# Kernel tuning notes

Measured on AMD Instinct MI355X. Metric: run time of the kernel, lower is better.

## Reference

```python
import jax, jax.numpy as jnp
import numpy as np
import math

FACTOR = 1

def setup_inputs() -> dict:
    key = jax.random.key(0)
    k1, k2, k3 = jax.random.split(key, 3)
    B, L, H, E = 32, 1024, 8, 64
    return {
        "queries": jax.random.normal(k1, (B, L, H, E), dtype=jnp.float32),
        "keys": jax.random.normal(k2, (B, L, H, E), dtype=jnp.float32),
        "values": jax.random.normal(k3, (B, L, H, E), dtype=jnp.float32),
        "attn_mask": 0,
    }


def reference(queries, keys, values, attn_mask):
    # queries/keys/values: [B, L, H, E] (S == L so no pad/truncate needed)
    B, L, H, E = queries.shape
    q = jnp.transpose(queries, (0, 2, 3, 1))  # [B,H,E,L]
    k = jnp.transpose(keys, (0, 2, 3, 1))
    v = jnp.transpose(values, (0, 2, 3, 1))   # [B,H,D,L]

    # FFT cross-correlation
    q_fft = jnp.fft.rfft(q, axis=-1)
    k_fft = jnp.fft.rfft(k, axis=-1)
    corr = jnp.fft.irfft(q_fft * jnp.conj(k_fft), n=L, axis=-1)  # [B,H,E,L]

    # top-k delay selection (global over batch, as in source)
    top_k = min(int(FACTOR * math.log(L)), L // 4, 32)  # static: 6
    mean_value = corr.mean(axis=(1, 2))                 # [B,L]
    weights, indices = jax.lax.top_k(mean_value.mean(axis=0), top_k)  # [k]
    tmp_corr = jax.nn.softmax(weights)                  # [k]

    # weighted circular-shift aggregation: roll(v, -indices[i]) summed with tmp_corr[i]
    pos = (jnp.arange(L)[None, :] + indices[:, None]) % L  # [k,L]
    patterns = v[:, :, :, pos]                              # [B,H,D,k,L]
    delays_agg = jnp.einsum('k,bhdkl->bhdl', tmp_corr, patterns)

    return jnp.transpose(delays_agg, (0, 3, 1, 2))  # [B,L,H,D]
```

## Files before the change

kernel.cpp:

```cpp
#include <hip/hip_runtime.h>
#include <math.h>

#define L_SEQ 1024
#define TOPK 6
#define SSTR 1057
#define NFBLK 2048

__device__ constexpr float TW32R[16] = {
  1.f, 0.98078528f, 0.92387953f, 0.83146961f, 0.70710678f, 0.55557023f,
  0.38268343f, 0.19509032f, 0.f, -0.19509032f, -0.38268343f, -0.55557023f,
  -0.70710678f, -0.83146961f, -0.92387953f, -0.98078528f};
__device__ constexpr float TW32I[16] = {
  0.f, -0.19509032f, -0.38268343f, -0.55557023f, -0.70710678f, -0.83146961f,
  -0.92387953f, -0.98078528f, -1.f, -0.98078528f, -0.92387953f, -0.83146961f,
  -0.70710678f, -0.55557023f, -0.38268343f, -0.19509032f};

#define FFTSTAGE(M, H, SH)                                                \
  _Pragma("unroll")                                                       \
  for (int k_ = 0; k_ < 32; k_ += (M)) {                                  \
    _Pragma("unroll")                                                     \
    for (int t_ = 0; t_ < (H); ++t_) {                                    \
      const int a_ = k_ + t_, b_ = a_ + (H);                              \
      const int m_ = t_ << (SH);                                          \
      float vr_, vi_;                                                     \
      if (m_ == 0)      { vr_ = zr[b_]; vi_ = zi[b_]; }                   \
      else if (m_ == 8) { vr_ = zi[b_]; vi_ = -zr[b_]; }                  \
      else {                                                              \
        vr_ = zr[b_] * TW32R[m_] - zi[b_] * TW32I[m_];                    \
        vi_ = zr[b_] * TW32I[m_] + zi[b_] * TW32R[m_];                    \
      }                                                                   \
      zr[b_] = zr[a_] - vr_; zi[b_] = zi[a_] - vi_;                       \
      zr[a_] += vr_;         zi[a_] += vi_;                               \
    }                                                                     \
  }

__global__ __launch_bounds__(256, 2) void fft_spec_kernel(
    const float* __restrict__ q, const float* __restrict__ k,
    float* __restrict__ partial)
{
  __shared__ float pr[8 * SSTR];
  __shared__ float pim[8 * SSTR];

  const int tid = threadIdx.x;
  const int bid = blockIdx.x;

  const int wq  = bid >> 3;
  const int xcd = bid & 7;
  const int octet = (wq & 1) | (((wq >> 1) & 3) << 1);
  const int h = (wq >> 3) & 7;
  const int b = (xcd << 2) | (wq >> 6);

  const float* qb = q + (size_t)b * 524288 + h * 64 + octet * 8;
  const float* kb = k + (size_t)b * 524288 + h * 64 + octet * 8;

  {
    const int ep = (tid & 1) * 4;
    const int lb = tid >> 1;
    const int col0 = (lb & 31) * 33 + (lb >> 5);
    #pragma unroll
    for (int it = 0; it < 8; ++it) {
      const int l = it * 128 + lb;
      const float4 qv = *(const float4*)(qb + (size_t)l * 512 + ep);
      const float4 kv = *(const float4*)(kb + (size_t)l * 512 + ep);
      const int col = col0 + it * 4;
      pr[(ep + 0) * SSTR + col] = qv.x;
      pr[(ep + 1) * SSTR + col] = qv.y;
      pr[(ep + 2) * SSTR + col] = qv.z;
      pr[(ep + 3) * SSTR + col] = qv.w;
      pim[(ep + 0) * SSTR + col] = kv.x;
      pim[(ep + 1) * SSTR + col] = kv.y;
      pim[(ep + 2) * SSTR + col] = kv.z;
      pim[(ep + 3) * SSTR + col] = kv.w;
    }
  }
  __syncthreads();

  const int s = tid >> 5;
  const int i = tid & 31;
  constexpr int BR[32] = {0,16,8,24,4,20,12,28,2,18,10,26,6,22,14,30,
                          1,17,9,25,5,21,13,29,3,19,11,27,7,23,15,31};
  const float astep = (float)i * 6.13592315e-03f;
  float zr[32], zi[32];

  {
    const int rowbase = s * SSTR + i * 33;
    #pragma unroll
    for (int p = 0; p < 32; ++p) {
      zr[p] = pr[rowbase + BR[p]];
      zi[p] = pim[rowbase + BR[p]];
    }
    FFTSTAGE(2, 1, 4) FFTSTAGE(4, 2, 3) FFTSTAGE(8, 4, 2)
    FFTSTAGE(16, 8, 1) FFTSTAGE(32, 16, 0)
    #pragma unroll
    for (int k2 = 0; k2 < 32; ++k2) {
      if (k2 == 0) {
        pr[rowbase]  = zr[0];
        pim[rowbase] = zi[0];
      } else {
        float sa, ca;
        __sincosf(astep * (float)k2, &sa, &ca);
        pr[rowbase + k2]  = zr[k2] * ca + zi[k2] * sa;
        pim[rowbase + k2] = zi[k2] * ca - zr[k2] * sa;
      }
    }
  }
  __syncthreads();

  const int j = i;
  #pragma unroll
  for (int p = 0; p < 32; ++p) {
    zr[p] = pr[s * SSTR + BR[p] * 33 + j];
    zi[p] = pim[s * SSTR + BR[p] * 33 + j];
  }
  __syncthreads();
  FFTSTAGE(2, 1, 4) FFTSTAGE(4, 2, 3) FFTSTAGE(8, 4, 2)
  FFTSTAGE(16, 8, 1) FFTSTAGE(32, 16, 0)

  {
    const int t64 = tid & 63;
    const int pl = (t64 & 32) | ((32 - j) & 31);
    #pragma unroll
    for (int k1 = 0; k1 < 32; ++k1) {
      float xr = __shfl(zr[31 - k1], pl, 64);
      float xi = __shfl(zi[31 - k1], pl, 64);
      if (j == 0) { xr = zr[(32 - k1) & 31]; xi = zi[(32 - k1) & 31]; }
      const float ar = zr[k1], ai = zi[k1];
      pr [s * SSTR + j * 33 + k1] = 0.5f  * (ar * xi + ai * xr);
      pim[s * SSTR + j * 33 + k1] = 0.25f * (ar * ar + ai * ai
                                             - xr * xr - xi * xi);
    }
  }
  __syncthreads();

  #pragma unroll
  for (int u = 0; u < 8; ++u) {
    const int bin = u * 256 + tid;
    const int bb = bin & 1023;
    const int jj = bb & 31, kk = bb >> 5;
    const float* pl_ = (u >= 4) ? pim : pr;
    float acc = 0.f;
    #pragma unroll
    for (int s2 = 0; s2 < 8; ++s2) acc += pl_[s2 * SSTR + jj * 33 + kk];
    partial[(size_t)bid * 2048 + bin] = acc;
  }
}

__global__ __launch_bounds__(256) void spec_reduce(
    const float* __restrict__ partial, float* __restrict__ S)
{
  const int t = threadIdx.x;
  const int b64 = t & 63, rc = t >> 6;
  const int v = blockIdx.x * 64 + b64;
  float acc = 0.f;
  for (int rr = rc * 512; rr < rc * 512 + 512; ++rr)
    acc += partial[(size_t)rr * 2048 + v];
  __shared__ float sm[4][65];
  sm[rc][b64] = acc;
  __syncthreads();
  if (t < 64)
    S[v] = sm[0][t] + sm[1][t] + sm[2][t] + sm[3][t];
}

__global__ __launch_bounds__(256) void corr_kernel(
    const float* __restrict__ S, float* __restrict__ c)
{
  __shared__ float sm[8][33];
  const int t = threadIdx.x;
  const int tau = blockIdx.x * 32 + (t & 31);
  const int jc = t >> 5;
  float acc = 0.f;
  #pragma unroll 4
  for (int jj = 0; jj < 128; ++jj) {
    const int j = jc * 128 + jj;
    float s_, c_;
    __sincosf((float)((j * tau) & 1023) * 6.13592315e-03f, &s_, &c_);
    acc += S[j] * c_ - S[1024 + j] * s_;
  }
  sm[jc][t & 31] = acc;
  __syncthreads();
  if (t < 32) {
    float r = 0.f;
    #pragma unroll
    for (int g = 0; g < 8; ++g) r += sm[g][t];
    c[blockIdx.x * 32 + t] = r * (1.0f / 16777216.0f);
  }
}

__global__ __launch_bounds__(256) void topk_kernel(
    const float* __restrict__ c, int* __restrict__ idx_out,
    float* __restrict__ w_out)
{
  __shared__ float vals[L_SEQ];
  __shared__ float rv[256];
  __shared__ int ri[256];
  __shared__ float topv[TOPK];
  __shared__ int topi[TOPK];
  const int tid = threadIdx.x;
  for (int i = tid; i < L_SEQ; i += 256) vals[i] = c[i];
  __syncthreads();

  for (int kk = 0; kk < TOPK; ++kk) {
    float bv = -INFINITY;
    int bi = 1 << 30;
    for (int i = tid; i < L_SEQ; i += 256) {
      const float v = vals[i];
      if (v > bv || (v == bv && i < bi)) { bv = v; bi = i; }
    }
    rv[tid] = bv; ri[tid] = bi;
    __syncthreads();
    for (int off = 128; off > 0; off >>= 1) {
      if (tid < off) {
        const float v2 = rv[tid + off];
        const int i2 = ri[tid + off];
        if (v2 > rv[tid] || (v2 == rv[tid] && i2 < ri[tid])) {
          rv[tid] = v2; ri[tid] = i2;
        }
      }
      __syncthreads();
    }
    if (tid == 0) {
      topv[kk] = rv[0];
      topi[kk] = ri[0];
      vals[ri[0]] = -INFINITY;
    }
    __syncthreads();
  }

  if (tid == 0) {
    const float m = topv[0];
    float e[TOPK], sum = 0.f;
    for (int i = 0; i < TOPK; ++i) { e[i] = expf(topv[i] - m); sum += e[i]; }
    const float inv = 1.0f / sum;
    for (int i = 0; i < TOPK; ++i) { w_out[i] = e[i] * inv; idx_out[i] = topi[i]; }
  }
}

__global__ __launch_bounds__(256) void agg_kernel(
    const float* __restrict__ v, const int* __restrict__ idx,
    const float* __restrict__ w, float4* __restrict__ out)
{
  __shared__ int sidx[TOPK];
  __shared__ float sw[TOPK];
  if (threadIdx.x < TOPK) {
    sidx[threadIdx.x] = idx[threadIdx.x];
    sw[threadIdx.x] = w[threadIdx.x];
  }
  __syncthreads();

  const int i = blockIdx.x * 256 + threadIdx.x;
  const int he4 = i & 127;
  const int l = (i >> 7) & (L_SEQ - 1);
  const int b = i >> 17;
  const float4* vb = (const float4*)v + (size_t)b * (L_SEQ * 128);

  float4 acc = make_float4(0.f, 0.f, 0.f, 0.f);
  #pragma unroll
  for (int kk = 0; kk < TOPK; ++kk) {
    const int src = (l + sidx[kk]) & (L_SEQ - 1);
    const float4 vv = vb[(size_t)src * 128 + he4];
    const float wk = sw[kk];
    acc.x += wk * vv.x; acc.y += wk * vv.y;
    acc.z += wk * vv.z; acc.w += wk * vv.w;
  }
  out[i] = acc;
}

extern "C" void kernel_launch(void* const* d_in, const int* in_sizes, int n_in,
                              void* d_out, int out_size, void* d_ws, size_t ws_size,
                              hipStream_t stream) {
  const float* q = (const float*)d_in[0];
  const float* k = (const float*)d_in[1];
  const float* v = (const float*)d_in[2];

  float* out = (float*)d_out;
  float* partial = out;

  float* c    = (float*)d_ws;
  int*   idxp = (int*)((char*)d_ws + 4096);
  float* wp   = (float*)((char*)d_ws + 4096 + 64);
  float* S    = (float*)((char*)d_ws + 8192);

  fft_spec_kernel<<<NFBLK, 256, 0, stream>>>(q, k, partial);
  spec_reduce<<<32, 256, 0, stream>>>(partial, S);
  corr_kernel<<<32, 256, 0, stream>>>(S, c);
  topk_kernel<<<1, 256, 0, stream>>>(c, idxp, wp);
  agg_kernel<<<(L_SEQ * 32 * 128) / 256, 256, 0, stream>>>(v, idxp, wp,
                                                           (float4*)out);
}
```

Measured before the change: 124.5 us.

## Pad FFT shared layout for float4 LDS access and split spectrum reduction wider

```diff
diff --git a/kernel.cpp b/kernel.cpp
--- a/kernel.cpp
+++ b/kernel.cpp
@@ -3,7 +3,8 @@
 
 #define L_SEQ 1024
 #define TOPK 6
-#define SSTR 1057
+#define RSTR 36
+#define PSTR 1156
 #define NFBLK 2048
 
 __device__ constexpr float TW32R[16] = {
@@ -38,8 +39,8 @@
     const float* __restrict__ q, const float* __restrict__ k,
     float* __restrict__ partial)
 {
-  __shared__ float pr[8 * SSTR];
-  __shared__ float pim[8 * SSTR];
+  __shared__ float pr[8 * PSTR];
+  __shared__ float pim[8 * PSTR];
 
   const int tid = threadIdx.x;
   const int bid = blockIdx.x;
@@ -56,21 +57,22 @@
   {
     const int ep = (tid & 1) * 4;
     const int lb = tid >> 1;
-    const int col0 = (lb & 31) * 33 + (lb >> 5);
+    const int r  = lb & 31;
+    const int cb = lb >> 5;
     #pragma unroll
     for (int it = 0; it < 8; ++it) {
       const int l = it * 128 + lb;
       const float4 qv = *(const float4*)(qb + (size_t)l * 512 + ep);
       const float4 kv = *(const float4*)(kb + (size_t)l * 512 + ep);
-      const int col = col0 + it * 4;
-      pr[(ep + 0) * SSTR + col] = qv.x;
-      pr[(ep + 1) * SSTR + col] = qv.y;
-      pr[(ep + 2) * SSTR + col] = qv.z;
-      pr[(ep + 3) * SSTR + col] = qv.w;
-      pim[(ep + 0) * SSTR + col] = kv.x;
-      pim[(ep + 1) * SSTR + col] = kv.y;
-      pim[(ep + 2) * SSTR + col] = kv.z;
-      pim[(ep + 3) * SSTR + col] = kv.w;
+      const int w = r * RSTR + cb + it * 4;
+      pr [(ep + 0) * PSTR + w] = qv.x;
+      pr [(ep + 1) * PSTR + w] = qv.y;
+      pr [(ep + 2) * PSTR + w] = qv.z;
+      pr [(ep + 3) * PSTR + w] = qv.w;
+      pim[(ep + 0) * PSTR + w] = kv.x;
+      pim[(ep + 1) * PSTR + w] = kv.y;
+      pim[(ep + 2) * PSTR + w] = kv.z;
+      pim[(ep + 3) * PSTR + w] = kv.w;
     }
   }
   __syncthreads();
@@ -83,98 +85,160 @@
   float zr[32], zi[32];
 
   {
-    const int rowbase = s * SSTR + i * 33;
-    #pragma unroll
-    for (int p = 0; p < 32; ++p) {
-      zr[p] = pr[rowbase + BR[p]];
-      zi[p] = pim[rowbase + BR[p]];
-    }
+    const int rowbase = s * PSTR + i * RSTR;
+    float lr[32], li[32];
+    #pragma unroll
+    for (int m = 0; m < 8; ++m) {
+      const float4 vr = *(const float4*)(pr  + rowbase + m * 4);
+      const float4 vi = *(const float4*)(pim + rowbase + m * 4);
+      lr[m*4+0] = vr.x; lr[m*4+1] = vr.y; lr[m*4+2] = vr.z; lr[m*4+3] = vr.w;
+      li[m*4+0] = vi.x; li[m*4+1] = vi.y; li[m*4+2] = vi.z; li[m*4+3] = vi.w;
+    }
+    #pragma unroll
+    for (int p = 0; p < 32; ++p) { zr[p] = lr[BR[p]]; zi[p] = li[BR[p]]; }
+
     FFTSTAGE(2, 1, 4) FFTSTAGE(4, 2, 3) FFTSTAGE(8, 4, 2)
     FFTSTAGE(16, 8, 1) FFTSTAGE(32, 16, 0)
-    #pragma unroll
-    for (int k2 = 0; k2 < 32; ++k2) {
-      if (k2 == 0) {
-        pr[rowbase]  = zr[0];
-        pim[rowbase] = zi[0];
-      } else {
-        float sa, ca;
-        __sincosf(astep * (float)k2, &sa, &ca);
-        pr[rowbase + k2]  = zr[k2] * ca + zi[k2] * sa;
-        pim[rowbase + k2] = zi[k2] * ca - zr[k2] * sa;
-      }
+
+    #pragma unroll
+    for (int k2 = 1; k2 < 32; ++k2) {
+      float sa, ca;
+      __sincosf(astep * (float)k2, &sa, &ca);
+      const float nr = zr[k2] * ca + zi[k2] * sa;
+      const float ni = zi[k2] * ca - zr[k2] * sa;
+      zr[k2] = nr; zi[k2] = ni;
+    }
+    #pragma unroll
+    for (int m = 0; m < 8; ++m) {
+      *(float4*)(pr  + rowbase + m * 4) =
+          make_float4(zr[m*4], zr[m*4+1], zr[m*4+2], zr[m*4+3]);
+      *(float4*)(pim + rowbase + m * 4) =
+          make_float4(zi[m*4], zi[m*4+1], zi[m*4+2], zi[m*4+3]);
     }
   }
   __syncthreads();
 
   const int j = i;
-  #pragma unroll
-  for (int p = 0; p < 32; ++p) {
-    zr[p] = pr[s * SSTR + BR[p] * 33 + j];
-    zi[p] = pim[s * SSTR + BR[p] * 33 + j];
-  }
-  __syncthreads();
+  {
+    float lr[32], li[32];
+    #pragma unroll
+    for (int r = 0; r < 32; ++r) {
+      lr[r] = pr [s * PSTR + r * RSTR + j];
+      li[r] = pim[s * PSTR + r * RSTR + j];
+    }
+    #pragma unroll
+    for (int p = 0; p < 32; ++p) { zr[p] = lr[BR[p]]; zi[p] = li[BR[p]]; }
+  }
+  __syncthreads();
+
   FFTSTAGE(2, 1, 4) FFTSTAGE(4, 2, 3) FFTSTAGE(8, 4, 2)
   FFTSTAGE(16, 8, 1) FFTSTAGE(32, 16, 0)
 
   {
     const int t64 = tid & 63;
     const int pl = (t64 & 32) | ((32 - j) & 31);
-    #pragma unroll
-    for (int k1 = 0; k1 < 32; ++k1) {
+    const int prow = s * PSTR + j * RSTR;
+    float sr_[16], si_[16];
+
+    #pragma unroll
+    for (int k1 = 0; k1 < 16; ++k1) {
       float xr = __shfl(zr[31 - k1], pl, 64);
       float xi = __shfl(zi[31 - k1], pl, 64);
       if (j == 0) { xr = zr[(32 - k1) & 31]; xi = zi[(32 - k1) & 31]; }
       const float ar = zr[k1], ai = zi[k1];
-      pr [s * SSTR + j * 33 + k1] = 0.5f  * (ar * xi + ai * xr);
-      pim[s * SSTR + j * 33 + k1] = 0.25f * (ar * ar + ai * ai
-                                             - xr * xr - xi * xi);
-    }
-  }
-  __syncthreads();
-
+      sr_[k1] = 0.5f  * (ar * xi + ai * xr);
+      si_[k1] = 0.25f * (ar * ar + ai * ai - xr * xr - xi * xi);
+    }
+    #pragma unroll
+    for (int m = 0; m < 4; ++m) {
+      *(float4*)(pr  + prow + m * 4) =
+          make_float4(sr_[m*4], sr_[m*4+1], sr_[m*4+2], sr_[m*4+3]);
+      *(float4*)(pim + prow + m * 4) =
+          make_float4(si_[m*4], si_[m*4+1], si_[m*4+2], si_[m*4+3]);
+    }
+
+    #pragma unroll
+    for (int k1 = 16; k1 < 32; ++k1) {
+      float xr = __shfl(zr[31 - k1], pl, 64);
+      float xi = __shfl(zi[31 - k1], pl, 64);
+      if (j == 0) { xr = zr[(32 - k1) & 31]; xi = zi[(32 - k1) & 31]; }
+      const float ar = zr[k1], ai = zi[k1];
+      sr_[k1 - 16] = 0.5f  * (ar * xi + ai * xr);
+      si_[k1 - 16] = 0.25f * (ar * ar + ai * ai - xr * xr - xi * xi);
+    }
+    #pragma unroll
+    for (int m = 0; m < 4; ++m) {
+      *(float4*)(pr  + prow + 16 + m * 4) =
+          make_float4(sr_[m*4], sr_[m*4+1], sr_[m*4+2], sr_[m*4+3]);
+      *(float4*)(pim + prow + 16 + m * 4) =
+          make_float4(si_[m*4], si_[m*4+1], si_[m*4+2], si_[m*4+3]);
+    }
+  }
+  __syncthreads();
+
+  {
+    const int jj = tid >> 3;
+    const int kq = tid & 7;
+    float arx = 0.f, ary = 0.f, arz = 0.f, arw = 0.f;
+    float aix = 0.f, aiy = 0.f, aiz = 0.f, aiw = 0.f;
+    #pragma unroll
+    for (int s2 = 0; s2 < 8; ++s2) {
+      const float4 vr = *(const float4*)(pr  + s2 * PSTR + jj * RSTR + kq * 4);
+      const float4 vi = *(const float4*)(pim + s2 * PSTR + jj * RSTR + kq * 4);
+      arx += vr.x; ary += vr.y; arz += vr.z; arw += vr.w;
+      aix += vi.x; aiy += vi.y; aiz += vi.z; aiw += vi.w;
+    }
+    const int v = jj * 32 + kq * 4;
+    *(float4*)(partial + (size_t)bid * 2048 + v) =
+        make_float4(arx, ary, arz, arw);
+    *(float4*)(partial + (size_t)bid * 2048 + 1024 + v) =
+        make_float4(aix, aiy, aiz, aiw);
+  }
+}
+
+__global__ __launch_bounds__(256) void spec_reduce(
+    const float* __restrict__ partial, float* __restrict__ S4)
+{
+  const int t = threadIdx.x;
+  const int b64 = t & 63, rq = t >> 6;
+  const int vb = (blockIdx.x & 31) * 64;
+  const int rc = blockIdx.x >> 5;
+  const int v = vb + b64;
+  float acc = 0.f;
+  const int r0 = rc * 512 + rq * 128;
+  for (int rr = r0; rr < r0 + 128; ++rr)
+    acc += partial[(size_t)rr * 2048 + v];
+  __shared__ float sm[4][65];
+  sm[rq][b64] = acc;
+  __syncthreads();
+  if (t < 64)
+    S4[(size_t)rc * 2048 + vb + t] =
+        sm[0][t] + sm[1][t] + sm[2][t] + sm[3][t];
+}
+
+__global__ __launch_bounds__(256) void corr_kernel(
+    const float* __restrict__ S4, float* __restrict__ c)
+{
+  __shared__ float Sr[2048];
+  __shared__ float sm[8][33];
+  const int t = threadIdx.x;
   #pragma unroll
   for (int u = 0; u < 8; ++u) {
-    const int bin = u * 256 + tid;
-    const int bb = bin & 1023;
-    const int jj = bb & 31, kk = bb >> 5;
-    const float* pl_ = (u >= 4) ? pim : pr;
-    float acc = 0.f;
-    #pragma unroll
-    for (int s2 = 0; s2 < 8; ++s2) acc += pl_[s2 * SSTR + jj * 33 + kk];
-    partial[(size_t)bid * 2048 + bin] = acc;
-  }
-}
-
-__global__ __launch_bounds__(256) void spec_reduce(
-    const float* __restrict__ partial, float* __restrict__ S)
-{
-  const int t = threadIdx.x;
-  const int b64 = t & 63, rc = t >> 6;
-  const int v = blockIdx.x * 64 + b64;
-  float acc = 0.f;
-  for (int rr = rc * 512; rr < rc * 512 + 512; ++rr)
-    acc += partial[(size_t)rr * 2048 + v];
-  __shared__ float sm[4][65];
-  sm[rc][b64] = acc;
-  __syncthreads();
-  if (t < 64)
-    S[v] = sm[0][t] + sm[1][t] + sm[2][t] + sm[3][t];
-}
-
-__global__ __launch_bounds__(256) void corr_kernel(
-    const float* __restrict__ S, float* __restrict__ c)
-{
-  __shared__ float sm[8][33];
-  const int t = threadIdx.x;
+    const int v = u * 256 + t;
+    Sr[v] = S4[v] + S4[2048 + v] + S4[4096 + v] + S4[6144 + v];
+  }
+  __syncthreads();
+
   const int tau = blockIdx.x * 32 + (t & 31);
   const int jc = t >> 5;
   float acc = 0.f;
   #pragma unroll 4
   for (int jj = 0; jj < 128; ++jj) {
-    const int j = jc * 128 + jj;
+    const int v = jc * 128 + jj;
+    const int jt = ((v & 31) << 5) | (v >> 5);
     float s_, c_;
-    __sincosf((float)((j * tau) & 1023) * 6.13592315e-03f, &s_, &c_);
-    acc += S[j] * c_ - S[1024 + j] * s_;
+    __sincosf((float)((jt * tau) & 1023) * 6.13592315e-03f, &s_, &c_);
+    acc += Sr[v] * c_ - Sr[1024 + v] * s_;
   }
   sm[jc][t & 31] = acc;
   __syncthreads();
@@ -274,15 +338,15 @@
 
   float* out = (float*)d_out;
   float* partial = out;
+  float* S4 = out + (size_t)8388608;
 
   float* c    = (float*)d_ws;
   int*   idxp = (int*)((char*)d_ws + 4096);
   float* wp   = (float*)((char*)d_ws + 4096 + 64);
-  float* S    = (float*)((char*)d_ws + 8192);
 
   fft_spec_kernel<<<NFBLK, 256, 0, stream>>>(q, k, partial);
-  spec_reduce<<<32, 256, 0, stream>>>(partial, S);
-  corr_kernel<<<32, 256, 0, stream>>>(S, c);
+  spec_reduce<<<128, 256, 0, stream>>>(partial, S4);
+  corr_kernel<<<32, 256, 0, stream>>>(S4, c);
   topk_kernel<<<1, 256, 0, stream>>>(c, idxp, wp);
   agg_kernel<<<(L_SEQ * 32 * 128) / 256, 256, 0, stream>>>(v, idxp, wp,
                                                            (float4*)out);
```

New measurement: 135.5 us. +8.8%, slower.
